# Kernel tuning notes

Measured on AMD Instinct MI355X. Metric: run time of the kernel, lower is better.

The kernel has to match this reference:

```python
import jax, jax.numpy as jnp
import numpy as np


def _onedirectional_dist(a, b):
    # a: [B, Na], b: [B, Nb] -> sum over Na of nearest-neighbor squared distance
    d2 = (a[:, :, None] - b[:, None, :]) ** 2          # [B, Na, Nb]
    d2 = jnp.where(jnp.isfinite(d2), d2, jnp.inf)      # mask non-finite -> inf
    nn_d2 = jnp.min(d2, axis=2)                        # [B, Na]
    nn_d2 = jnp.where(jnp.isfinite(nn_d2), nn_d2, 0.0) # all-inf rows -> 0
    return nn_d2.sum(axis=1)                           # [B]


def setup_inputs() -> dict:
    key = jax.random.key(0)
    k1, k2 = jax.random.split(key)
    # B=1 (the torch broadcast target/target_max only works for B==1 w/o mask)
    target = jax.random.uniform(k1, (1, 1, 480, 640), jnp.float32, 0.1, 10.0)
    bin_centers = jax.random.uniform(k2, (1, 256), jnp.float32, 0.1, 10.0)
    return {"target": target, "bin_centers": bin_centers}


def reference(target, bin_centers):
    # scale_invariant=True, mask=None path
    target_max = jnp.max(target, axis=(2, 3))       # [B, 1]
    bin_centers_max = jnp.max(bin_centers, axis=1)  # [B]
    target_n = target / target_max                  # per-image normalization (B==1)
    bin_centers_n = bin_centers / bin_centers_max
    target_depths = target_n.reshape(target_n.shape[0], -1)  # [B, H*W]
    bidir = _onedirectional_dist(bin_centers_n, target_depths) \
          + _onedirectional_dist(target_depths, bin_centers_n)
    return bidir.mean()
```

## Files before the change

kernel.cpp:

```cpp
#include <hip/hip_runtime.h>
#include <math.h>

#define THREADS 256
#define BPB 8
#define PCH 16
#define TMAXB 128


__device__ __forceinline__ float wmaxAll(float v) {
  #pragma unroll
  for (int o = 32; o > 0; o >>= 1) v = fmaxf(v, __shfl_xor(v, o, 64));
  return v;
}
__device__ __forceinline__ float wminAll(float v) {
  #pragma unroll
  for (int o = 32; o > 0; o >>= 1) v = fminf(v, __shfl_xor(v, o, 64));
  return v;
}
__device__ __forceinline__ float wsumAll(float v) {
  #pragma unroll
  for (int o = 32; o > 0; o >>= 1) v += __shfl_xor(v, o, 64);
  return v;
}
__device__ __forceinline__ double wsumAllD(double v) {
  #pragma unroll
  for (int o = 32; o > 0; o >>= 1) v += __shfl_xor(v, o, 64);
  return v;
}

__device__ __forceinline__ unsigned keyEnc(float f) {
  unsigned u = __float_as_uint(f);
  return (u & 0x80000000u) ? ~u : (u | 0x80000000u);
}
__device__ __forceinline__ float keyDec(unsigned k) {
  unsigned u = (k & 0x80000000u) ? (k ^ 0x80000000u) : ~k;
  return __uint_as_float(u);
}

__global__ __launch_bounds__(THREADS) void k_tmax(const float4* __restrict__ t4, int n4,
                                                  const float* __restrict__ t, int n,
                                                  const float* __restrict__ bins, int nb,
                                                  float* __restrict__ pmax,
                                                  float* __restrict__ bmax,
                                                  unsigned int* __restrict__ counter,
                                                  double* __restrict__ psumd,
                                                  unsigned int* __restrict__ binmin) {
  const int tid = threadIdx.x;
  const int lane = tid & 63, w = tid >> 6;
  float v = 0.0f;
  int idx = blockIdx.x * THREADS + tid;
  int stride = gridDim.x * THREADS;
  for (int i = idx; i < n4; i += stride) {
    float4 a = t4[i];
    v = fmaxf(v, fmaxf(fmaxf(a.x, a.y), fmaxf(a.z, a.w)));
  }
  for (int i = n4 * 4 + idx; i < n; i += stride) v = fmaxf(v, t[i]);
  v = wmaxAll(v);
  if (lane == 0) pmax[blockIdx.x * 4 + w] = v;

  if (blockIdx.x == 0) {
    for (int i = tid; i < 256; i += THREADS) binmin[i] = 0xFFFFFFFFu;
    if (tid < 8) psumd[tid * 8] = 0.0;
    if (tid == 0) *counter = 0u;
    if (w == 0) {
      float bv = 0.0f;
      for (int i = lane; i < nb; i += 64) bv = fmaxf(bv, bins[i]);
      bv = wmaxAll(bv);
      if (lane == 0) *bmax = bv;
    }
  }
}

__global__ __launch_bounds__(THREADS) void k_main(const float4* __restrict__ t4, int n4,
                                                  const float* __restrict__ t, int n,
                                                  const float* __restrict__ bins, int nb,
                                                  const float* __restrict__ pmax,
                                                  const float* __restrict__ bmax,
                                                  double* __restrict__ psumd,
                                                  unsigned int* __restrict__ binmin,
                                                  unsigned int* __restrict__ counter,
                                                  float* __restrict__ out,
                                                  int nt2, int G) {
  __shared__ float sb[256], hb[256];
  __shared__ float sm1[4 * BPB];
  __shared__ float ss[4];
  __shared__ double ds[4];
  __shared__ unsigned int ticket;

  const int tid = threadIdx.x;
  const int lane = tid & 63, w = tid >> 6;
  const int bid = blockIdx.x;

  float v = 0.0f;
  for (int i = lane; i < TMAXB * 4; i += 64) v = fmaxf(v, pmax[i]);
  const float it = 1.0f / wmaxAll(v);
  const float ib = 1.0f / *bmax;

  if (bid < nt2) {
    for (int i = tid; i < nb && i < 256; i += THREADS) {
      float b = bins[i] * ib;
      sb[i] = b * b;
      hb[i] = -(b + b);
    }
    __syncthreads();
    float lsum = 0.0f;
    int idx = bid * THREADS + tid;
    if (idx < n4) {
      float4 a = t4[idx];
      float t0 = a.x * it, t1 = a.y * it, t2 = a.z * it, t3 = a.w * it;
      float m0 = 1e30f, m1 = 1e30f, m2 = 1e30f, m3 = 1e30f;
      #pragma unroll 8
      for (int j = 0; j < nb; j++) {
        float s = sb[j], h = hb[j];
        m0 = fminf(m0, fmaf(h, t0, s));
        m1 = fminf(m1, fmaf(h, t1, s));
        m2 = fminf(m2, fmaf(h, t2, s));
        m3 = fminf(m3, fmaf(h, t3, s));
      }
      lsum = (fmaf(t0, t0, m0) + fmaf(t1, t1, m1)) + (fmaf(t2, t2, m2) + fmaf(t3, t3, m3));
    }
    int ntail = n - n4 * 4;
    if (bid == 0 && tid < ntail) {
      float tv = t[n4 * 4 + tid] * it;
      float m = 1e30f;
      for (int j = 0; j < nb; j++) m = fminf(m, fmaf(hb[j], tv, sb[j]));
      lsum += fmaf(tv, tv, m);
    }
    float s = wsumAll(lsum);
    if (lane == 0) ss[w] = s;
    __syncthreads();
    if (tid == 0)
      atomicAdd(&psumd[(bid & 7) * 8], (double)((ss[0] + ss[1]) + (ss[2] + ss[3])));
  } else {
    const int b1 = bid - nt2;
    const int g = b1 / PCH, c = b1 % PCH;
    const int base = g * BPB;
    float bn[BPB], mn[BPB];
    #pragma unroll
    for (int k = 0; k < BPB; k++) {
      int bi = base + k;
      bn[k] = (bi < nb) ? bins[bi] * ib : 3e30f;
      mn[k] = 1e30f;
    }
    const int chunk = (n4 + PCH - 1) / PCH;
    const int lo = c * chunk;
    const int hi = (lo + chunk < n4) ? lo + chunk : n4;
    for (int i = lo + tid; i < hi; i += THREADS) {
      float4 a = t4[i];
      float t0 = a.x * it, t1 = a.y * it, t2 = a.z * it, t3 = a.w * it;
      float s0 = t0 * t0, s1 = t1 * t1, s2 = t2 * t2, s3 = t3 * t3;
      float h0 = -(t0 + t0), h1 = -(t1 + t1), h2 = -(t2 + t2), h3 = -(t3 + t3);
      #pragma unroll
      for (int k = 0; k < BPB; k++) {
        float b = bn[k];
        mn[k] = fminf(mn[k], fmaf(h0, b, s0));
        mn[k] = fminf(mn[k], fmaf(h1, b, s1));
        mn[k] = fminf(mn[k], fmaf(h2, b, s2));
        mn[k] = fminf(mn[k], fmaf(h3, b, s3));
      }
    }
    int ntail = n - n4 * 4;
    if (c == 0 && tid < ntail) {
      float tv = t[n4 * 4 + tid] * it;
      float s = tv * tv, h = -(tv + tv);
      #pragma unroll
      for (int k = 0; k < BPB; k++) mn[k] = fminf(mn[k], fmaf(h, bn[k], s));
    }
    #pragma unroll
    for (int k = 0; k < BPB; k++) {
      float m = wminAll(mn[k]);
      if (lane == 0) sm1[w * BPB + k] = m;
    }
    __syncthreads();
    if (tid < BPB && base + tid < nb) {
      float m = fminf(fminf(sm1[tid], sm1[BPB + tid]),
                      fminf(sm1[2 * BPB + tid], sm1[3 * BPB + tid]));
      atomicMin(&binmin[base + tid], keyEnc(m));
    }
  }

  asm volatile("s_waitcnt vmcnt(0)" ::: "memory");
  if (tid == 0) ticket = atomicAdd(counter, 1u);
  __syncthreads();
  if (ticket == (unsigned int)(G - 1)) {
    double tsum = 0.0;
    for (int b = tid; b < nb; b += THREADS) {
      float m = keyDec(binmin[b]);
      float bnv = bins[b] * ib;
      float val = fmaf(bnv, bnv, m);
      tsum += (m < 1e29f) ? (double)val : 0.0;
    }
    if (tid < 8) tsum += psumd[tid * 8];
    tsum = wsumAllD(tsum);
    if (lane == 0) ds[w] = tsum;
    __syncthreads();
    if (tid == 0) out[0] = (float)((ds[0] + ds[1]) + (ds[2] + ds[3]));
  }
}

extern "C" void kernel_launch(void* const* d_in, const int* in_sizes, int n_in,
                              void* d_out, int out_size, void* d_ws, size_t ws_size,
                              hipStream_t stream) {
  const float* target = (const float*)d_in[0];
  const float* bins = (const float*)d_in[1];
  const int n = in_sizes[0];
  const int nb = in_sizes[1];
  float* out = (float*)d_out;

  unsigned int* counter = (unsigned int*)d_ws;
  float* bmax = (float*)((char*)d_ws + 64);
  float* pmax = (float*)((char*)d_ws + 256);
  double* psumd = (double*)((char*)d_ws + 2560);
  unsigned int* binmin = (unsigned int*)((char*)d_ws + 4096);

  const int n4 = n / 4;
  const float4* t4 = (const float4*)target;

  k_tmax<<<TMAXB, THREADS, 0, stream>>>(t4, n4, target, n, bins, nb,
                                        pmax, bmax, counter, psumd, binmin);

  const int nt2 = (n4 + THREADS - 1) / THREADS;
  const int nt1 = ((nb + BPB - 1) / BPB) * PCH;
  const int G = nt2 + nt1;
  k_main<<<G, THREADS, 0, stream>>>(t4, n4, target, n, bins, nb, pmax, bmax,
                                    psumd, binmin, counter, out, nt2, G);
}
```

Measured before the change: 76.19 us.

## Fuse target-max reduction into main kernel with a spin-wait grid flag

Moves the global max-of-target reduction into the main kernel. The bin-side blocks compute partial maxima, the last one to finish publishes the inverse max through a flag, and the pixel-side blocks prefetch their data and then spin on that flag. A tiny init kernel replaces the old 128-block max kernel, so the heavy reduction no longer sits in its own launch. This relies on every block being co-resident, because the spin-wait can deadlock if they are not, and the waiting blocks hold compute resources while they spin.

```diff
diff --git a/kernel.cpp b/kernel.cpp
--- a/kernel.cpp
+++ b/kernel.cpp
@@ -4,7 +4,6 @@
 #define THREADS 256
 #define BPB 8
 #define PCH 16
-#define TMAXB 128
 
 
 __device__ __forceinline__ float wmaxAll(float v) {
@@ -37,77 +36,76 @@
   return __uint_as_float(u);
 }
 
-__global__ __launch_bounds__(THREADS) void k_tmax(const float4* __restrict__ t4, int n4,
-                                                  const float* __restrict__ t, int n,
-                                                  const float* __restrict__ bins, int nb,
-                                                  float* __restrict__ pmax,
-                                                  float* __restrict__ bmax,
-                                                  unsigned int* __restrict__ counter,
-                                                  double* __restrict__ psumd,
-                                                  unsigned int* __restrict__ binmin) {
+__device__ __forceinline__ unsigned aload(const unsigned* p) {
+  return __hip_atomic_load(p, __ATOMIC_RELAXED, __HIP_MEMORY_SCOPE_AGENT);
+}
+__device__ __forceinline__ void astore(unsigned* p, unsigned v) {
+  __hip_atomic_store(p, v, __ATOMIC_RELAXED, __HIP_MEMORY_SCOPE_AGENT);
+}
+
+__global__ __launch_bounds__(64) void k_init(const float* __restrict__ bins, int nb,
+                                             unsigned* __restrict__ c0,
+                                             unsigned* __restrict__ c1,
+                                             unsigned* __restrict__ go,
+                                             float* __restrict__ bmax,
+                                             double* __restrict__ psumd,
+                                             unsigned* __restrict__ binmin) {
   const int tid = threadIdx.x;
-  const int lane = tid & 63, w = tid >> 6;
-  float v = 0.0f;
-  int idx = blockIdx.x * THREADS + tid;
-  int stride = gridDim.x * THREADS;
-  for (int i = idx; i < n4; i += stride) {
-    float4 a = t4[i];
-    v = fmaxf(v, fmaxf(fmaxf(a.x, a.y), fmaxf(a.z, a.w)));
-  }
-  for (int i = n4 * 4 + idx; i < n; i += stride) v = fmaxf(v, t[i]);
-  v = wmaxAll(v);
-  if (lane == 0) pmax[blockIdx.x * 4 + w] = v;
-
-  if (blockIdx.x == 0) {
-    for (int i = tid; i < 256; i += THREADS) binmin[i] = 0xFFFFFFFFu;
-    if (tid < 8) psumd[tid * 8] = 0.0;
-    if (tid == 0) *counter = 0u;
-    if (w == 0) {
-      float bv = 0.0f;
-      for (int i = lane; i < nb; i += 64) bv = fmaxf(bv, bins[i]);
-      bv = wmaxAll(bv);
-      if (lane == 0) *bmax = bv;
-    }
-  }
-}
-
-__global__ __launch_bounds__(THREADS) void k_main(const float4* __restrict__ t4, int n4,
-                                                  const float* __restrict__ t, int n,
-                                                  const float* __restrict__ bins, int nb,
-                                                  const float* __restrict__ pmax,
-                                                  const float* __restrict__ bmax,
-                                                  double* __restrict__ psumd,
-                                                  unsigned int* __restrict__ binmin,
-                                                  unsigned int* __restrict__ counter,
-                                                  float* __restrict__ out,
-                                                  int nt2, int G) {
+  for (int i = tid; i < nb; i += 64) binmin[i] = 0xFFFFFFFFu;
+  if (tid < 8) psumd[tid * 8] = 0.0;
+  if (tid == 0) { *c0 = 0u; *c1 = 0u; *go = 0u; }
+  float bv = 0.0f;
+  for (int i = tid; i < nb; i += 64) bv = fmaxf(bv, bins[i]);
+  bv = wmaxAll(bv);
+  if (tid == 0) *bmax = bv;
+}
+
+__global__ __launch_bounds__(THREADS) void k_fused(const float4* __restrict__ t4, int n4,
+                                                   const float* __restrict__ t, int n,
+                                                   const float* __restrict__ bins, int nb,
+                                                   unsigned* __restrict__ c0,
+                                                   unsigned* __restrict__ c1,
+                                                   unsigned* __restrict__ go,
+                                                   const float* __restrict__ bmaxp,
+                                                   unsigned* __restrict__ pmax,
+                                                   double* __restrict__ psumd,
+                                                   unsigned* __restrict__ binmin,
+                                                   float* __restrict__ out,
+                                                   int NT2, int G1, int G) {
+  __shared__ float sred[4];
   __shared__ float sb[256], hb[256];
   __shared__ float sm1[4 * BPB];
   __shared__ float ss[4];
   __shared__ double ds[4];
-  __shared__ unsigned int ticket;
+  __shared__ unsigned sold, sgo, sticket;
 
   const int tid = threadIdx.x;
   const int lane = tid & 63, w = tid >> 6;
   const int bid = blockIdx.x;
-
-  float v = 0.0f;
-  for (int i = lane; i < TMAXB * 4; i += 64) v = fmaxf(v, pmax[i]);
-  const float it = 1.0f / wmaxAll(v);
-  const float ib = 1.0f / *bmax;
-
-  if (bid < nt2) {
+  const int ntail = n - n4 * 4;
+  const float ibf = 1.0f / *bmaxp;
+
+  if (bid < NT2) {
+    const int idx = bid * THREADS + tid;
+    float4 a = make_float4(0.f, 0.f, 0.f, 0.f);
+    const bool has = (idx < n4);
+    if (has) a = t4[idx];
     for (int i = tid; i < nb && i < 256; i += THREADS) {
-      float b = bins[i] * ib;
+      float b = bins[i] * ibf;
       sb[i] = b * b;
       hb[i] = -(b + b);
     }
-    __syncthreads();
+    if (tid == 0) {
+      unsigned gv;
+      while ((gv = aload(go)) == 0u) __builtin_amdgcn_s_sleep(4);
+      sgo = gv;
+    }
+    __syncthreads();
+    const float itf = __uint_as_float(sgo);
+
     float lsum = 0.0f;
-    int idx = bid * THREADS + tid;
-    if (idx < n4) {
-      float4 a = t4[idx];
-      float t0 = a.x * it, t1 = a.y * it, t2 = a.z * it, t3 = a.w * it;
+    if (has) {
+      float t0 = a.x * itf, t1 = a.y * itf, t2 = a.z * itf, t3 = a.w * itf;
       float m0 = 1e30f, m1 = 1e30f, m2 = 1e30f, m3 = 1e30f;
       #pragma unroll 8
       for (int j = 0; j < nb; j++) {
@@ -119,9 +117,8 @@
       }
       lsum = (fmaf(t0, t0, m0) + fmaf(t1, t1, m1)) + (fmaf(t2, t2, m2) + fmaf(t3, t3, m3));
     }
-    int ntail = n - n4 * 4;
     if (bid == 0 && tid < ntail) {
-      float tv = t[n4 * 4 + tid] * it;
+      float tv = t[n4 * 4 + tid] * itf;
       float m = 1e30f;
       for (int j = 0; j < nb; j++) m = fminf(m, fmaf(hb[j], tv, sb[j]));
       lsum += fmaf(tv, tv, m);
@@ -132,14 +129,54 @@
     if (tid == 0)
       atomicAdd(&psumd[(bid & 7) * 8], (double)((ss[0] + ss[1]) + (ss[2] + ss[3])));
   } else {
-    const int b1 = bid - nt2;
+    const int b1 = bid - NT2;
+    float v = 0.0f;
+    const int stride0 = G1 * THREADS;
+    for (int i = b1 * THREADS + tid; i < n4; i += stride0) {
+      float4 a = t4[i];
+      v = fmaxf(v, fmaxf(fmaxf(a.x, a.y), fmaxf(a.z, a.w)));
+    }
+    for (int i = n4 * 4 + b1 * THREADS + tid; i < n; i += stride0) v = fmaxf(v, t[i]);
+    v = wmaxAll(v);
+    if (lane == 0) sred[w] = v;
+    __syncthreads();
+    if (tid == 0) {
+      float p = fmaxf(fmaxf(sred[0], sred[1]), fmaxf(sred[2], sred[3]));
+      astore(&pmax[b1], __float_as_uint(p));
+      asm volatile("s_waitcnt vmcnt(0)" ::: "memory");
+      sold = atomicAdd(c0, 1u);
+    }
+    __syncthreads();
+    if (sold == (unsigned)(G1 - 1)) {
+      float m = 0.0f;
+      for (int i = tid; i < G1; i += THREADS) m = fmaxf(m, __uint_as_float(aload(&pmax[i])));
+      m = wmaxAll(m);
+      if (lane == 0) sred[w] = m;
+      __syncthreads();
+      if (tid == 0) {
+        float T = fmaxf(fmaxf(sred[0], sred[1]), fmaxf(sred[2], sred[3]));
+        unsigned gv = __float_as_uint(1.0f / T);
+        astore(go, gv);
+        sgo = gv;
+      }
+      __syncthreads();
+    } else {
+      if (tid == 0) {
+        unsigned gv;
+        while ((gv = aload(go)) == 0u) __builtin_amdgcn_s_sleep(4);
+        sgo = gv;
+      }
+      __syncthreads();
+    }
+    const float itf = __uint_as_float(sgo);
+
     const int g = b1 / PCH, c = b1 % PCH;
     const int base = g * BPB;
     float bn[BPB], mn[BPB];
     #pragma unroll
     for (int k = 0; k < BPB; k++) {
       int bi = base + k;
-      bn[k] = (bi < nb) ? bins[bi] * ib : 3e30f;
+      bn[k] = (bi < nb) ? bins[bi] * ibf : 3e30f;
       mn[k] = 1e30f;
     }
     const int chunk = (n4 + PCH - 1) / PCH;
@@ -147,7 +184,7 @@
     const int hi = (lo + chunk < n4) ? lo + chunk : n4;
     for (int i = lo + tid; i < hi; i += THREADS) {
       float4 a = t4[i];
-      float t0 = a.x * it, t1 = a.y * it, t2 = a.z * it, t3 = a.w * it;
+      float t0 = a.x * itf, t1 = a.y * itf, t2 = a.z * itf, t3 = a.w * itf;
       float s0 = t0 * t0, s1 = t1 * t1, s2 = t2 * t2, s3 = t3 * t3;
       float h0 = -(t0 + t0), h1 = -(t1 + t1), h2 = -(t2 + t2), h3 = -(t3 + t3);
       #pragma unroll
@@ -159,9 +196,8 @@
         mn[k] = fminf(mn[k], fmaf(h3, b, s3));
       }
     }
-    int ntail = n - n4 * 4;
     if (c == 0 && tid < ntail) {
-      float tv = t[n4 * 4 + tid] * it;
+      float tv = t[n4 * 4 + tid] * itf;
       float s = tv * tv, h = -(tv + tv);
       #pragma unroll
       for (int k = 0; k < BPB; k++) mn[k] = fminf(mn[k], fmaf(h, bn[k], s));
@@ -180,17 +216,18 @@
   }
 
   asm volatile("s_waitcnt vmcnt(0)" ::: "memory");
-  if (tid == 0) ticket = atomicAdd(counter, 1u);
+  if (tid == 0) sticket = atomicAdd(c1, 1u);
   __syncthreads();
-  if (ticket == (unsigned int)(G - 1)) {
+  if (sticket == (unsigned)(G - 1)) {
     double tsum = 0.0;
     for (int b = tid; b < nb; b += THREADS) {
-      float m = keyDec(binmin[b]);
-      float bnv = bins[b] * ib;
+      float m = keyDec(aload(&binmin[b]));
+      float bnv = bins[b] * ibf;
       float val = fmaf(bnv, bnv, m);
       tsum += (m < 1e29f) ? (double)val : 0.0;
     }
-    if (tid < 8) tsum += psumd[tid * 8];
+    if (tid < 8)
+      tsum += __hip_atomic_load(&psumd[tid * 8], __ATOMIC_RELAXED, __HIP_MEMORY_SCOPE_AGENT);
     tsum = wsumAllD(tsum);
     if (lane == 0) ds[w] = tsum;
     __syncthreads();
@@ -207,21 +244,23 @@
   const int nb = in_sizes[1];
   float* out = (float*)d_out;
 
-  unsigned int* counter = (unsigned int*)d_ws;
-  float* bmax = (float*)((char*)d_ws + 64);
-  float* pmax = (float*)((char*)d_ws + 256);
-  double* psumd = (double*)((char*)d_ws + 2560);
-  unsigned int* binmin = (unsigned int*)((char*)d_ws + 4096);
+  unsigned* c0 = (unsigned*)d_ws;
+  unsigned* c1 = (unsigned*)((char*)d_ws + 64);
+  unsigned* go = (unsigned*)((char*)d_ws + 128);
+  float* bmax = (float*)((char*)d_ws + 192);
+  double* psumd = (double*)((char*)d_ws + 2048);
+  unsigned* pmax = (unsigned*)((char*)d_ws + 4096);
+  unsigned* binmin = (unsigned*)((char*)d_ws + 8192);
 
   const int n4 = n / 4;
   const float4* t4 = (const float4*)target;
 
-  k_tmax<<<TMAXB, THREADS, 0, stream>>>(t4, n4, target, n, bins, nb,
-                                        pmax, bmax, counter, psumd, binmin);
-
-  const int nt2 = (n4 + THREADS - 1) / THREADS;
-  const int nt1 = ((nb + BPB - 1) / BPB) * PCH;
-  const int G = nt2 + nt1;
-  k_main<<<G, THREADS, 0, stream>>>(t4, n4, target, n, bins, nb, pmax, bmax,
-                                    psumd, binmin, counter, out, nt2, G);
-}
+  k_init<<<1, 64, 0, stream>>>(bins, nb, c0, c1, go, bmax, psumd, binmin);
+
+  const int NT2 = (n4 + THREADS - 1) / THREADS;
+  const int G1 = ((nb + BPB - 1) / BPB) * PCH;
+  const int G = NT2 + G1;
+  k_fused<<<G, THREADS, 0, stream>>>(t4, n4, target, n, bins, nb,
+                                     c0, c1, go, bmax, pmax, psumd, binmin,
+                                     out, NT2, G1, G);
+}
```

New measurement: 81.84 us. 1.07x slower.

## Fuse both nearest-neighbor directions into one block pass sharing staged target tile

Applied to the files above, without the earlier changes.

Drops the separate bin-side blocks that each re-read a chunk of the target. Each block now stages its 1024 normalized target values in shared memory. Its threads then compute both the target-to-bin minima and, with one thread per bin, the bin-to-target minima over that tile, followed by one atomicMin per bin per block. This removes the second full read of the target and the extra blocks, but adds a serial 1024-element shared-memory scan per thread and about 300 blocks times 256 atomicMins on the same 256 addresses.

```diff
diff --git a/kernel.cpp b/kernel.cpp
--- a/kernel.cpp
+++ b/kernel.cpp
@@ -2,19 +2,12 @@
 #include <math.h>
 
 #define THREADS 256
-#define BPB 8
-#define PCH 16
 #define TMAXB 128
 
 
 __device__ __forceinline__ float wmaxAll(float v) {
   #pragma unroll
   for (int o = 32; o > 0; o >>= 1) v = fmaxf(v, __shfl_xor(v, o, 64));
-  return v;
-}
-__device__ __forceinline__ float wminAll(float v) {
-  #pragma unroll
-  for (int o = 32; o > 0; o >>= 1) v = fminf(v, __shfl_xor(v, o, 64));
   return v;
 }
 __device__ __forceinline__ float wsumAll(float v) {
@@ -42,9 +35,9 @@
                                                   const float* __restrict__ bins, int nb,
                                                   float* __restrict__ pmax,
                                                   float* __restrict__ bmax,
-                                                  unsigned int* __restrict__ counter,
+                                                  unsigned* __restrict__ c1,
                                                   double* __restrict__ psumd,
-                                                  unsigned int* __restrict__ binmin) {
+                                                  unsigned* __restrict__ binmin) {
   const int tid = threadIdx.x;
   const int lane = tid & 63, w = tid >> 6;
   float v = 0.0f;
@@ -59,9 +52,9 @@
   if (lane == 0) pmax[blockIdx.x * 4 + w] = v;
 
   if (blockIdx.x == 0) {
-    for (int i = tid; i < 256; i += THREADS) binmin[i] = 0xFFFFFFFFu;
+    for (int i = tid; i < nb; i += THREADS) binmin[i] = 0xFFFFFFFFu;
     if (tid < 8) psumd[tid * 8] = 0.0;
-    if (tid == 0) *counter = 0u;
+    if (tid == 0) *c1 = 0u;
     if (w == 0) {
       float bv = 0.0f;
       for (int i = lane; i < nb; i += 64) bv = fmaxf(bv, bins[i]);
@@ -71,126 +64,114 @@
   }
 }
 
-__global__ __launch_bounds__(THREADS) void k_main(const float4* __restrict__ t4, int n4,
+__global__ __launch_bounds__(THREADS) void k_comb(const float4* __restrict__ t4, int n4,
                                                   const float* __restrict__ t, int n,
                                                   const float* __restrict__ bins, int nb,
                                                   const float* __restrict__ pmax,
-                                                  const float* __restrict__ bmax,
+                                                  const float* __restrict__ bmaxp,
                                                   double* __restrict__ psumd,
-                                                  unsigned int* __restrict__ binmin,
-                                                  unsigned int* __restrict__ counter,
-                                                  float* __restrict__ out,
-                                                  int nt2, int G) {
+                                                  unsigned* __restrict__ binmin,
+                                                  unsigned* __restrict__ c1,
+                                                  float* __restrict__ out, int G) {
   __shared__ float sb[256], hb[256];
-  __shared__ float sm1[4 * BPB];
+  __shared__ float tp[1024];
   __shared__ float ss[4];
   __shared__ double ds[4];
-  __shared__ unsigned int ticket;
+  __shared__ unsigned sticket;
 
   const int tid = threadIdx.x;
   const int lane = tid & 63, w = tid >> 6;
   const int bid = blockIdx.x;
+  const int ntail = n - n4 * 4;
 
   float v = 0.0f;
   for (int i = lane; i < TMAXB * 4; i += 64) v = fmaxf(v, pmax[i]);
-  const float it = 1.0f / wmaxAll(v);
-  const float ib = 1.0f / *bmax;
-
-  if (bid < nt2) {
-    for (int i = tid; i < nb && i < 256; i += THREADS) {
-      float b = bins[i] * ib;
-      sb[i] = b * b;
-      hb[i] = -(b + b);
-    }
-    __syncthreads();
-    float lsum = 0.0f;
-    int idx = bid * THREADS + tid;
-    if (idx < n4) {
-      float4 a = t4[idx];
-      float t0 = a.x * it, t1 = a.y * it, t2 = a.z * it, t3 = a.w * it;
-      float m0 = 1e30f, m1 = 1e30f, m2 = 1e30f, m3 = 1e30f;
-      #pragma unroll 8
-      for (int j = 0; j < nb; j++) {
-        float s = sb[j], h = hb[j];
-        m0 = fminf(m0, fmaf(h, t0, s));
-        m1 = fminf(m1, fmaf(h, t1, s));
-        m2 = fminf(m2, fmaf(h, t2, s));
-        m3 = fminf(m3, fmaf(h, t3, s));
-      }
-      lsum = (fmaf(t0, t0, m0) + fmaf(t1, t1, m1)) + (fmaf(t2, t2, m2) + fmaf(t3, t3, m3));
-    }
-    int ntail = n - n4 * 4;
-    if (bid == 0 && tid < ntail) {
-      float tv = t[n4 * 4 + tid] * it;
-      float m = 1e30f;
-      for (int j = 0; j < nb; j++) m = fminf(m, fmaf(hb[j], tv, sb[j]));
-      lsum += fmaf(tv, tv, m);
-    }
-    float s = wsumAll(lsum);
-    if (lane == 0) ss[w] = s;
-    __syncthreads();
-    if (tid == 0)
-      atomicAdd(&psumd[(bid & 7) * 8], (double)((ss[0] + ss[1]) + (ss[2] + ss[3])));
-  } else {
-    const int b1 = bid - nt2;
-    const int g = b1 / PCH, c = b1 % PCH;
-    const int base = g * BPB;
-    float bn[BPB], mn[BPB];
-    #pragma unroll
-    for (int k = 0; k < BPB; k++) {
-      int bi = base + k;
-      bn[k] = (bi < nb) ? bins[bi] * ib : 3e30f;
-      mn[k] = 1e30f;
-    }
-    const int chunk = (n4 + PCH - 1) / PCH;
-    const int lo = c * chunk;
-    const int hi = (lo + chunk < n4) ? lo + chunk : n4;
-    for (int i = lo + tid; i < hi; i += THREADS) {
-      float4 a = t4[i];
-      float t0 = a.x * it, t1 = a.y * it, t2 = a.z * it, t3 = a.w * it;
-      float s0 = t0 * t0, s1 = t1 * t1, s2 = t2 * t2, s3 = t3 * t3;
-      float h0 = -(t0 + t0), h1 = -(t1 + t1), h2 = -(t2 + t2), h3 = -(t3 + t3);
-      #pragma unroll
-      for (int k = 0; k < BPB; k++) {
-        float b = bn[k];
-        mn[k] = fminf(mn[k], fmaf(h0, b, s0));
-        mn[k] = fminf(mn[k], fmaf(h1, b, s1));
-        mn[k] = fminf(mn[k], fmaf(h2, b, s2));
-        mn[k] = fminf(mn[k], fmaf(h3, b, s3));
-      }
-    }
-    int ntail = n - n4 * 4;
-    if (c == 0 && tid < ntail) {
-      float tv = t[n4 * 4 + tid] * it;
-      float s = tv * tv, h = -(tv + tv);
-      #pragma unroll
-      for (int k = 0; k < BPB; k++) mn[k] = fminf(mn[k], fmaf(h, bn[k], s));
-    }
-    #pragma unroll
-    for (int k = 0; k < BPB; k++) {
-      float m = wminAll(mn[k]);
-      if (lane == 0) sm1[w * BPB + k] = m;
-    }
-    __syncthreads();
-    if (tid < BPB && base + tid < nb) {
-      float m = fminf(fminf(sm1[tid], sm1[BPB + tid]),
-                      fminf(sm1[2 * BPB + tid], sm1[3 * BPB + tid]));
-      atomicMin(&binmin[base + tid], keyEnc(m));
-    }
-  }
+  const float itf = 1.0f / wmaxAll(v);
+  const float ibf = 1.0f / *bmaxp;
+
+  for (int i = tid; i < nb && i < 256; i += THREADS) {
+    float b = bins[i] * ibf;
+    sb[i] = b * b;
+    hb[i] = -(b + b);
+  }
+
+  const int idx = bid * THREADS + tid;
+  const bool has = (idx < n4);
+  float t0 = 0.f, t1 = 0.f, t2 = 0.f, t3 = 0.f;
+  if (has) {
+    float4 a = t4[idx];
+    t0 = a.x * itf; t1 = a.y * itf; t2 = a.z * itf; t3 = a.w * itf;
+    *(float4*)&tp[tid * 4] = make_float4(t0, t1, t2, t3);
+  }
+  __syncthreads();
+
+  float lsum = 0.0f;
+  if (has) {
+    float m0 = 1e30f, m1 = 1e30f, m2 = 1e30f, m3 = 1e30f;
+    #pragma unroll 8
+    for (int j = 0; j < nb; j++) {
+      float s = sb[j], h = hb[j];
+      m0 = fminf(m0, fmaf(h, t0, s));
+      m1 = fminf(m1, fmaf(h, t1, s));
+      m2 = fminf(m2, fmaf(h, t2, s));
+      m3 = fminf(m3, fmaf(h, t3, s));
+    }
+    lsum = (fmaf(t0, t0, m0) + fmaf(t1, t1, m1)) + (fmaf(t2, t2, m2) + fmaf(t3, t3, m3));
+  }
+  if (bid == 0 && tid < ntail) {
+    float tv = t[n4 * 4 + tid] * itf;
+    float m = 1e30f;
+    for (int j = 0; j < nb; j++) m = fminf(m, fmaf(hb[j], tv, sb[j]));
+    lsum += fmaf(tv, tv, m);
+  }
+
+  const int nf4 = n4 - bid * THREADS;
+  const int P = 4 * (nf4 < THREADS ? (nf4 > 0 ? nf4 : 0) : THREADS);
+  float bnv = 0.f, mb2 = 0.f;
+  if (tid < nb) { bnv = bins[tid] * ibf; mb2 = -bnv * bnv; }
+  float ma = 1e30f, mb = 1e30f, mc = 1e30f, md = 1e30f;
+  for (int p = 0; p < P; p += 4) {
+    float4 q = *(const float4*)&tp[p];
+    float u0 = q.x - bnv, u1 = q.y - bnv, u2 = q.z - bnv, u3 = q.w - bnv;
+    ma = fminf(ma, fmaf(u0, u0, mb2));
+    mb = fminf(mb, fmaf(u1, u1, mb2));
+    mc = fminf(mc, fmaf(u2, u2, mb2));
+    md = fminf(md, fmaf(u3, u3, mb2));
+  }
+  if (bid == 0) {
+    for (int i = 0; i < ntail; i++) {
+      float tv = t[n4 * 4 + i] * itf;
+      float u = tv - bnv;
+      ma = fminf(ma, fmaf(u, u, mb2));
+    }
+  }
+  if (tid < nb) {
+    float bm = fminf(fminf(ma, mb), fminf(mc, md));
+    atomicMin(&binmin[tid], keyEnc(bm));
+  }
+
+  float s = wsumAll(lsum);
+  if (lane == 0) ss[w] = s;
+  __syncthreads();
+  if (tid == 0)
+    atomicAdd(&psumd[(bid & 7) * 8], (double)((ss[0] + ss[1]) + (ss[2] + ss[3])));
 
   asm volatile("s_waitcnt vmcnt(0)" ::: "memory");
-  if (tid == 0) ticket = atomicAdd(counter, 1u);
+  if (tid == 0) sticket = atomicAdd(c1, 1u);
   __syncthreads();
-  if (ticket == (unsigned int)(G - 1)) {
+  if (sticket == (unsigned)(G - 1)) {
     double tsum = 0.0;
     for (int b = tid; b < nb; b += THREADS) {
-      float m = keyDec(binmin[b]);
-      float bnv = bins[b] * ib;
-      float val = fmaf(bnv, bnv, m);
+      unsigned key = __hip_atomic_load(&binmin[b], __ATOMIC_RELAXED,
+                                       __HIP_MEMORY_SCOPE_AGENT);
+      float m = keyDec(key);
+      float bv = bins[b] * ibf;
+      float val = fmaf(bv, bv, m);
       tsum += (m < 1e29f) ? (double)val : 0.0;
     }
-    if (tid < 8) tsum += psumd[tid * 8];
+    if (tid < 8)
+      tsum += __hip_atomic_load(&psumd[tid * 8], __ATOMIC_RELAXED,
+                                __HIP_MEMORY_SCOPE_AGENT);
     tsum = wsumAllD(tsum);
     if (lane == 0) ds[w] = tsum;
     __syncthreads();
@@ -207,21 +188,19 @@
   const int nb = in_sizes[1];
   float* out = (float*)d_out;
 
-  unsigned int* counter = (unsigned int*)d_ws;
+  unsigned* c1 = (unsigned*)d_ws;
   float* bmax = (float*)((char*)d_ws + 64);
-  float* pmax = (float*)((char*)d_ws + 256);
-  double* psumd = (double*)((char*)d_ws + 2560);
-  unsigned int* binmin = (unsigned int*)((char*)d_ws + 4096);
+  float* pmax = (float*)((char*)d_ws + 1024);
+  double* psumd = (double*)((char*)d_ws + 4096);
+  unsigned* binmin = (unsigned*)((char*)d_ws + 8192);
 
   const int n4 = n / 4;
   const float4* t4 = (const float4*)target;
 
   k_tmax<<<TMAXB, THREADS, 0, stream>>>(t4, n4, target, n, bins, nb,
-                                        pmax, bmax, counter, psumd, binmin);
-
-  const int nt2 = (n4 + THREADS - 1) / THREADS;
-  const int nt1 = ((nb + BPB - 1) / BPB) * PCH;
-  const int G = nt2 + nt1;
-  k_main<<<G, THREADS, 0, stream>>>(t4, n4, target, n, bins, nb, pmax, bmax,
-                                    psumd, binmin, counter, out, nt2, G);
-}
+                                        pmax, bmax, c1, psumd, binmin);
+
+  const int G = (n4 + THREADS - 1) / THREADS;
+  k_comb<<<G, THREADS, 0, stream>>>(t4, n4, target, n, bins, nb, pmax, bmax,
+                                    psumd, binmin, c1, out, G);
+}
```

Result: slower. 89.86 us (+18.0%).
